# Kernel tuning notes

Measured on AMD Instinct MI355X. Metric: run time of the kernel, lower is better.

The kernel has to match this reference:

```python
import jax, jax.numpy as jnp
import numpy as np

P_THRESHOLD = 0.6
K_CAP = 16


def softmax_m1(x):
    # f(x) = (exp(x)-1) / sum(exp(x)-1), as in the torch module
    fx = jnp.expm1(x)
    return fx / fx.sum(-1, keepdims=True)


def align_chars(start_map, nb_map, max_ch):
    # eval-mode recurrence of NeighborDecoder.align_chars, run for a fixed
    # max_ch steps (no data-dependent early break; char_masks carry the
    # finished state exactly as in torch).
    b = start_map.shape[0]

    def step(carry, i):
        char_map, finished = carry  # [b, N+1], [b] int32
        mask = (finished == 0).astype(char_map.dtype)
        out = (char_map, mask)  # emitted BEFORE the update, matching torch
        finished = finished + (char_map[:, -1] > P_THRESHOLD).astype(jnp.int32)
        kk = jnp.minimum(1 + 2 * i, K_CAP).astype(char_map.dtype)
        cmd = softmax_m1(jax.lax.stop_gradient(char_map) * kk)  # .detach() in torch
        nxt = jnp.einsum('bn,bnm->bm', cmd, nb_map)
        return (nxt, finished), out

    init = (start_map, jnp.zeros(b, jnp.int32))
    _, (maps, masks) = jax.lax.scan(step, init, jnp.arange(max_ch))
    return maps.transpose(1, 0, 2), masks.T  # [b, T, N+1], [b, T]


def setup_inputs() -> dict:
    key = jax.random.key(0)
    ks = jax.random.split(key, 8)
    b, c, h, w = 32, 384, 16, 64
    num_classes = 97
    s = 1.0 / np.sqrt(c)
    return {
        'x': jax.random.normal(ks[0], (b, c, h, w), jnp.float32),
        'eos_emb': (jax.random.normal(ks[1], (c,), jnp.float32) * 0.02),
        'q_w': jax.random.normal(ks[2], (c, c), jnp.float32) * s,
        'q_b': jnp.zeros((c,), jnp.float32),
        'k_w': jax.random.normal(ks[3], (c, c), jnp.float32) * s,
        'k_b': jnp.zeros((c,), jnp.float32),
        'nav_w': jax.random.normal(ks[4], (1, c, c), jnp.float32) * 0.01,
        'nav_b': jnp.zeros((1,), jnp.float32),
        'cls_w': jax.random.normal(ks[5], (num_classes, c), jnp.float32) * s,
        'cls_b': jnp.zeros((num_classes,), jnp.float32),
        'max_char': 48,
    }


def reference(x, eos_emb, q_w, q_b, k_w, k_b, nav_w, nav_b, cls_w, cls_b, max_char):
    b, c, h, w = x.shape
    scale = float(c) ** 0.5
    xt = x.reshape(b, c, h * w).transpose(0, 2, 1)  # [b, N, c]
    g = xt.mean(axis=1)  # [b, c]
    x_ext = jnp.concatenate(
        [xt, jnp.broadcast_to(eos_emb, (b, 1, c))], axis=1)  # [b, N+1, c]

    q_start = g @ q_w.T + q_b                      # [b, c]
    k_feat = x_ext @ k_w.T + k_b                   # [b, N+1, c]
    start_map = jnp.einsum('bnc,bc->bn', k_feat, q_start) / scale
    start_map = jax.nn.softmax(start_map, axis=1)  # [b, N+1]

    q_feat = xt @ q_w.T + q_b                      # [b, N, c]
    # BilinearLayer with out=1: einsum('bim,mn,bjn->bij') + bias
    nb_map = jnp.einsum('bim,mn,bjn->bij', q_feat, nav_w[0], k_feat) + nav_b[0]
    nb_map = jax.nn.softmax(nb_map / scale, axis=2)  # [b, N, N+1]

    last = jnp.zeros((h * w + 1,), x.dtype).at[-1].set(1.0)
    nb_map = jnp.concatenate(
        [nb_map, jnp.broadcast_to(last, (b, 1, h * w + 1))], axis=1)  # [b, N+1, N+1]

    char_maps, char_masks = align_chars(start_map, nb_map, max_char)
    char_feats = jnp.einsum('btn,bnc->btc', char_maps, x_ext)
    char_feats = char_feats * char_masks[..., None]
    logits = char_feats @ cls_w.T + cls_b          # [b, T, num_classes]
    return logits, char_feats, char_maps, char_masks, nb_map
```

## Files before the change

### kernel.cpp

```cpp
#include <hip/hip_runtime.h>
#include <cstdint>
#include <cstddef>

#define BB   32
#define CC   384
#define NN   1024
#define N1   1025
#define TT   48
#define NCLS 97
#define NBL_LD 1088
#define NBTS   1056

static constexpr float INV_SCALE = 1.0f / 19.595917942265423f;

using bf16x8 = __attribute__((ext_vector_type(8))) __bf16;
using f32x4  = __attribute__((ext_vector_type(4))) float;

static constexpr size_t OFF_LOGITS = 0;
static constexpr size_t OFF_CFEAT  = 148992;
static constexpr size_t OFF_CMAPS  = 738816;
static constexpr size_t OFF_CMASK  = 2313216;
static constexpr size_t OFF_NB     = 2314752;

static constexpr size_t OFF_XB     = 0;
static constexpr size_t OFF_WGEM   = 25165824;
static constexpr size_t OFF_BIAS   = 25755648;
static constexpr size_t OFF_G      = 25758720;
static constexpr size_t OFF_QSTART = 25807872;
static constexpr size_t OFF_KEOS   = 25857024;
static constexpr size_t OFF_STATS  = 25858560;
static constexpr size_t OFF_MAPSBF = 26120704;
static constexpr size_t OFF_CMD    = 29266432;
static constexpr size_t OFF_PSUM   = 29536768;
static constexpr size_t OFF_XBT    = 29569536;
static constexpr size_t OFF_NBL    = 29569536;
static constexpr size_t OFF_OUT    = 100942336;
static constexpr size_t OFF_NBT    = 100942336;

__device__ __forceinline__ float bf2f(uint u) {
    union { uint i; float f; } v; v.i = u << 16; return v.f;
}
__device__ __forceinline__ ushort f2bf(float f) {
    union { float f; uint i; } v; v.f = f;
    uint r = v.i + 0x7fffu + ((v.i >> 16) & 1u);
    return (ushort)(r >> 16);
}

__device__ __forceinline__ void gld16(const ushort* g, ushort* l) {
    __builtin_amdgcn_global_load_lds(
        (const __attribute__((address_space(1))) uint*)g,
        (__attribute__((address_space(3))) uint*)l, 16, 0, 0);
}

__global__ __launch_bounds__(256) void k_conv_mean(
    const float* __restrict__ x, ushort* __restrict__ xb, float* __restrict__ g)
{
    int row  = blockIdx.x * 4 + (threadIdx.x >> 6);
    int lane = threadIdx.x & 63;
    const float* src = x + (size_t)row * NN;
    ushort* dst = xb + (size_t)row * NN;
    float s = 0.f;
#pragma unroll
    for (int q = 0; q < 4; q++) {
        float4 v = ((const float4*)src)[q * 64 + lane];
        s += v.x + v.y + v.z + v.w;
        ushort4 p; p.x = f2bf(v.x); p.y = f2bf(v.y); p.z = f2bf(v.z); p.w = f2bf(v.w);
        ((ushort4*)dst)[q * 64 + lane] = p;
    }
#pragma unroll
    for (int o = 32; o; o >>= 1) s += __shfl_down(s, o);
    if (lane == 0) g[row] = s * (1.0f / NN);
}

__global__ __launch_bounds__(256) void k_transpose(
    const ushort* __restrict__ xb, ushort* __restrict__ xbT)
{
    int b = blockIdx.z, c0 = blockIdx.x * 64, n0 = blockIdx.y * 64;
    __shared__ ushort t[64][65];
    int ur = threadIdx.x >> 5, uc = threadIdx.x & 31;
    const ushort* src = xb + ((size_t)b * CC + c0) * NN + n0;
#pragma unroll
    for (int p = 0; p < 8; p++) {
        int c = p * 8 + ur;
        uint v = ((const uint*)(src + (size_t)c * NN))[uc];
        t[c][uc * 2]     = (ushort)(v & 0xffffu);
        t[c][uc * 2 + 1] = (ushort)(v >> 16);
    }
    __syncthreads();
    ushort* dst = xbT + ((size_t)b * N1 + n0) * CC + c0;
#pragma unroll
    for (int p = 0; p < 8; p++) {
        int n = p * 8 + ur;
        uint v = (uint)t[uc * 2][n] | (((uint)t[uc * 2 + 1][n]) << 16);
        ((uint*)(dst + (size_t)n * CC))[uc] = v;
    }
}

__global__ __launch_bounds__(384) void k_setup(
    const float* __restrict__ k_w, const float* __restrict__ k_b,
    const float* __restrict__ nav_w, const float* __restrict__ q_w,
    const float* __restrict__ q_b, const float* __restrict__ eos,
    const float* __restrict__ g,
    ushort* __restrict__ Wgem, float* __restrict__ bias,
    ushort* __restrict__ xbT, float* __restrict__ keos,
    ushort* __restrict__ Out, float* __restrict__ q_start)
{
    int blk = blockIdx.x, c = threadIdx.x;
    if (blk < 384) {
        Wgem[(size_t)blk * CC + c] = f2bf(k_w[(size_t)blk * CC + c]);
        if (c == 0) bias[blk] = k_b[blk];
    } else if (blk < 768) {
        int m = blk - 384;
        float acc = 0.f, accb = 0.f;
        for (int k = 0; k < CC; k++) {
            float nv = nav_w[(size_t)k * CC + m];
            acc  += nv * q_w[(size_t)k * CC + c];
            accb += nv * q_b[k];
        }
        Wgem[(size_t)(CC + m) * CC + c] = f2bf(acc);
        if (c == 0) bias[CC + m] = accb;
    } else if (blk < 800) {
        int b = blk - 768;
        xbT[((size_t)b * N1 + NN) * CC + c] = f2bf(eos[c]);
    } else if (blk == 800) {
        float acc = k_b[c];
        const float* w = k_w + (size_t)c * CC;
        for (int k = 0; k < CC; k++) acc += eos[k] * w[k];
        keos[c] = acc;
        ushort v = f2bf(acc);
        for (int b = 0; b < BB; b++) Out[((size_t)b * N1 + NN) * 768 + c] = v;
    } else {
        int b = blk - 801;
        __shared__ float gs[CC];
        gs[c] = g[(size_t)b * CC + c];
        __syncthreads();
        float acc = q_b[c];
        const float* w = q_w + (size_t)c * CC;
        for (int k = 0; k < CC; k++) acc += gs[k] * w[k];
        q_start[(size_t)b * CC + c] = acc;
    }
}

template<int MODE, int NTN, int PERB>
__global__ __launch_bounds__(256) void k_gemm(
    const ushort* __restrict__ Aall, size_t strideAb, int lda,
    const ushort* __restrict__ Ball, size_t strideBb, int ldb,
    ushort* __restrict__ Cout, size_t strideCb, int ldc,
    const float* __restrict__ bias)
{
    int wid = blockIdx.x;
    int xcd = wid & 7;
    int work = xcd * (PERB * 4) + (wid >> 3);
    int b = work / PERB;
    int r = work - b * PERB;
    int m0 = (r / NTN) * 128, n0 = (r % NTN) * 128;

    const ushort* A  = Aall + (size_t)b * strideAb;
    const ushort* Bp = Ball + (size_t)b * strideBb;
    __shared__ ushort sbuf[16384];
    ushort* As = sbuf;
    ushort* Bs = sbuf + 8192;
    int tid = threadIdx.x, wave = tid >> 6, lane = tid & 63;
    int wm = wave >> 1, wn = wave & 1;
    f32x4 acc[4][4] = {};

    for (int k0 = 0; k0 < CC; k0 += 64) {
#pragma unroll
        for (int q = 0; q < 4; q++) {
            int idx = q * 256 + tid, rr = idx >> 3, sw = idx & 7;
            int src = (sw ^ (rr & 7)) << 3;
            ushort* dA = As + (size_t)(q * 2048 + wave * 512);
            ushort* dB = Bs + (size_t)(q * 2048 + wave * 512);
            gld16(A  + (size_t)(m0 + rr) * lda + k0 + src, dA);
            gld16(Bp + (size_t)(n0 + rr) * ldb + k0 + src, dB);
        }
        __syncthreads();
#pragma unroll
        for (int h = 0; h < 2; h++) {
            bf16x8 af[4], bfr[4];
            int chb = h * 4 + (lane >> 4);
#pragma unroll
            for (int i = 0; i < 4; i++) {
                int row = wm * 64 + i * 16 + (lane & 15);
                af[i]  = *(const bf16x8*)(As + row * 64 + ((chb ^ (row & 7)) << 3));
                int col = wn * 64 + i * 16 + (lane & 15);
                bfr[i] = *(const bf16x8*)(Bs + col * 64 + ((chb ^ (col & 7)) << 3));
            }
#pragma unroll
            for (int i = 0; i < 4; i++)
#pragma unroll
                for (int j = 0; j < 4; j++)
                    acc[i][j] = __builtin_amdgcn_mfma_f32_16x16x32_bf16(af[i], bfr[j], acc[i][j], 0, 0, 0);
        }
        __syncthreads();
    }
#pragma unroll
    for (int i = 0; i < 4; i++) {
        int rl = wm * 64 + i * 16 + ((lane >> 4) << 2);
#pragma unroll
        for (int j = 0; j < 4; j++) {
            int cl = wn * 64 + j * 16 + (lane & 15);
            float bv = (MODE == 0) ? bias[n0 + cl] : 0.f;
#pragma unroll
            for (int rr = 0; rr < 4; rr++) {
                float val = (MODE == 0) ? (acc[i][j][rr] + bv) : (acc[i][j][rr] * INV_SCALE);
                sbuf[(rl + rr) * 128 + cl] = f2bf(val);
            }
        }
    }
    __syncthreads();
    ushort* Cb = Cout + (size_t)b * strideCb;
#pragma unroll
    for (int q = 0; q < 8; q++) {
        int idx = q * 256 + tid, row = idx >> 4, seg = idx & 15;
        *(uint4*)(Cb + (size_t)(m0 + row) * ldc + n0 + seg * 8) =
            *(const uint4*)(sbuf + row * 128 + seg * 8);
    }
}

__global__ __launch_bounds__(1024) void k_start(
    const ushort* __restrict__ Out, const float* __restrict__ q_start,
    float* __restrict__ cmaps)
{
    int b = blockIdx.x, tid = threadIdx.x;
    __shared__ float qs[CC];
    __shared__ float red[16];
    __shared__ float bc;
    if (tid < CC) qs[tid] = q_start[(size_t)b * CC + tid];
    __syncthreads();
    auto dot = [&](int n) {
        const uint4* row = (const uint4*)(Out + ((size_t)b * N1 + n) * 768);
        float acc = 0.f;
        for (int c8 = 0; c8 < CC / 8; c8++) {
            uint4 u = row[c8];
            const ushort* us = (const ushort*)&u;
#pragma unroll
            for (int e = 0; e < 8; e++) acc += bf2f(us[e]) * qs[c8 * 8 + e];
        }
        return acc * INV_SCALE;
    };
    float v0 = dot(tid);
    float v1 = (tid == 0) ? dot(1024) : -1e30f;
    float lm = fmaxf(v0, v1);
#pragma unroll
    for (int o = 32; o; o >>= 1) lm = fmaxf(lm, __shfl_down(lm, o));
    if ((tid & 63) == 0) red[tid >> 6] = lm;
    __syncthreads();
    if (tid == 0) { float m = red[0]; for (int i = 1; i < 16; i++) m = fmaxf(m, red[i]); bc = m; }
    __syncthreads();
    float bmax = bc;
    float e0 = __expf(v0 - bmax);
    float e1 = (tid == 0) ? __expf(v1 - bmax) : 0.f;
    float ls = e0 + e1;
#pragma unroll
    for (int o = 32; o; o >>= 1) ls += __shfl_down(ls, o);
    if ((tid & 63) == 0) red[tid >> 6] = ls;
    __syncthreads();
    if (tid == 0) { float s = 0.f; for (int i = 0; i < 16; i++) s += red[i]; bc = s; }
    __syncthreads();
    float inv = 1.f / bc;
    float* o = cmaps + ((size_t)b * TT) * N1;
    o[tid] = e0 * inv;
    if (tid == 0) o[1024] = e1 * inv;
}

__global__ __launch_bounds__(256) void k_eoscol_nbl(
    const ushort* __restrict__ Out, const float* __restrict__ keos, ushort* __restrict__ nbL)
{
    int gw = blockIdx.x * 4 + (threadIdx.x >> 6);
    int lane = threadIdx.x & 63;
    for (int rr = 0; rr < 4; rr++) {
        int gi = gw * 4 + rr, b = gi >> 10, i = gi & 1023;
        const ushort* row = Out + ((size_t)b * N1 + i) * 768 + 384;
        float acc = 0.f;
        for (int c = lane; c < CC; c += 64) acc += bf2f(row[c]) * keos[c];
#pragma unroll
        for (int o = 32; o; o >>= 1) acc += __shfl_down(acc, o);
        if (lane == 0) nbL[((size_t)b * N1 + i) * NBL_LD + 1024] = f2bf(acc * INV_SCALE);
    }
}

__global__ __launch_bounds__(256) void k_softnb2(
    const ushort* __restrict__ nbL, float* __restrict__ nb, float2* __restrict__ stats)
{
    int bi = blockIdx.x;
    int b = bi >> 10, i = bi & 1023;
    const ushort* row = nbL + ((size_t)b * N1 + i) * NBL_LD;
    int tid = threadIdx.x;
    uint2 u = *(const uint2*)(row + tid * 4);
    float v0 = bf2f(u.x & 0xffffu), v1 = bf2f(u.x >> 16);
    float v2 = bf2f(u.y & 0xffffu), v3 = bf2f(u.y >> 16);
    float vt = (tid == 0) ? bf2f(row[1024]) : -1e30f;
    __shared__ float r1[4]; __shared__ float bc;
    float lm = fmaxf(fmaxf(fmaxf(v0, v1), fmaxf(v2, v3)), vt);
#pragma unroll
    for (int o = 32; o; o >>= 1) lm = fmaxf(lm, __shfl_down(lm, o));
    if ((tid & 63) == 0) r1[tid >> 6] = lm;
    __syncthreads();
    if (tid == 0) bc = fmaxf(fmaxf(r1[0], r1[1]), fmaxf(r1[2], r1[3]));
    __syncthreads();
    float m = bc;
    float e0 = __expf(v0 - m), e1 = __expf(v1 - m), e2 = __expf(v2 - m), e3 = __expf(v3 - m);
    float et = (tid == 0) ? __expf(vt - m) : 0.f;
    float s = e0 + e1 + e2 + e3 + et;
#pragma unroll
    for (int o = 32; o; o >>= 1) s += __shfl_down(s, o);
    if ((tid & 63) == 0) r1[tid >> 6] = s;
    __syncthreads();
    if (tid == 0) bc = r1[0] + r1[1] + r1[2] + r1[3];
    __syncthreads();
    float inv = 1.f / bc;
    float* orow = nb + ((size_t)b * N1 + i) * N1;
    float4 ov = make_float4(e0 * inv, e1 * inv, e2 * inv, e3 * inv);
    *(float4*)(orow + tid * 4) = ov;
    if (tid == 0) { orow[1024] = et * inv; stats[b * 1024 + i] = make_float2(m, inv); }
}

__global__ void k_onehot(float* __restrict__ nb)
{
    int b = blockIdx.x;
    float* row = nb + ((size_t)b * N1 + NN) * N1;
    for (int j = threadIdx.x; j < N1; j += 256)
        row[j] = (j == 1024) ? 1.f : 0.f;
}

__global__ __launch_bounds__(256) void k_transq(
    const ushort* __restrict__ nbL, const float2* __restrict__ stats,
    ushort* __restrict__ nbT)
{
    int b = blockIdx.z, n0 = blockIdx.x * 64, j0 = blockIdx.y * 64;
    __shared__ ushort tile[64][80];
    __shared__ float2 st[64];
    int tid = threadIdx.x;
    if (tid < 64) st[tid] = stats[b * 1024 + n0 + tid];
    __syncthreads();
#pragma unroll
    for (int q = 0; q < 2; q++) {
        int idx = q * 256 + tid, rl = idx >> 3, ch = idx & 7;
        const ushort* src = nbL + ((size_t)b * N1 + n0 + rl) * NBL_LD + j0 + ch * 8;
        uint4 u = *(const uint4*)src;
        float2 s = st[rl];
        const ushort* us = (const ushort*)&u;
#pragma unroll
        for (int k = 0; k < 8; k++)
            tile[ch * 8 + k][rl] = f2bf(__expf(bf2f(us[k]) - s.x) * s.y);
    }
    __syncthreads();
#pragma unroll
    for (int q = 0; q < 2; q++) {
        int idx = q * 256 + tid, jl = idx >> 3, seg = idx & 7;
        int j = j0 + jl;
        if (j <= 1024) {
            uint4 v = *(const uint4*)&tile[jl][seg * 8];
            *(uint4*)(nbT + ((size_t)b * N1 + j) * NBTS + n0 + seg * 8) = v;
        }
    }
}

__global__ __launch_bounds__(256) void k_cmd0(
    const float* __restrict__ cmaps, float* __restrict__ cmd_out, float* __restrict__ ps_out)
{
    int b = blockIdx.x, tid = threadIdx.x;
    __shared__ float red[4];
    const float* m = cmaps + (size_t)b * TT * N1;
    float s = 0.f;
    for (int n = tid; n < N1; n += 256) {
        float c = expm1f(m[n]);
        cmd_out[(size_t)b * 1056 + n] = c;
        s += c;
    }
#pragma unroll
    for (int o = 32; o; o >>= 1) s += __shfl_down(s, o);
    if ((tid & 63) == 0) red[tid >> 6] = s;
    __syncthreads();
    if (tid == 0) ps_out[b * 128] = red[0] + red[1] + red[2] + red[3];
    else if (tid < 128) ps_out[b * 128 + tid] = 0.f;
}

__device__ __forceinline__ float dot16(uint4 r0, uint4 r1,
                                       const float* cA, const float* cB)
{
    const ushort* p0 = (const ushort*)&r0;
    const ushort* p1 = (const ushort*)&r1;
    float acc = 0.f;
#pragma unroll
    for (int e = 0; e < 8; e++) acc += bf2f(p0[e]) * cA[e];
#pragma unroll
    for (int e = 0; e < 8; e++) acc += bf2f(p1[e]) * cB[e];
    return acc;
}

__global__ __launch_bounds__(256) void k_step4(
    float* __restrict__ cmaps, const ushort* __restrict__ nbT,
    const float* __restrict__ cmd_in, float* __restrict__ cmd_out,
    const float* __restrict__ ps_in, float* __restrict__ ps_out, int t)
{
    int b = blockIdx.y, blk = blockIdx.x;
    int tid = threadIdx.x, wave = tid >> 6, lane = tid & 63;
    int j0 = blk * 32 + wave * 8;
    const ushort* base = nbT + (size_t)b * N1 * NBTS;

    uint4 rv[8][2];
#pragma unroll
    for (int r = 0; r < 8; ++r) {
        int j = j0 + r; if (j > 1024) j = 1024;
        const ushort* row = base + (size_t)j * NBTS;
        rv[r][0] = *(const uint4*)(row + lane * 8);
        rv[r][1] = *(const uint4*)(row + 512 + lane * 8);
    }
    const float* ci = cmd_in + (size_t)b * 1056;
    float cA[8], cB[8];
    *(float4*)&cA[0] = *(const float4*)(ci + lane * 8);
    *(float4*)&cA[4] = *(const float4*)(ci + lane * 8 + 4);
    *(float4*)&cB[0] = *(const float4*)(ci + 512 + lane * 8);
    *(float4*)&cB[4] = *(const float4*)(ci + 512 + lane * 8 + 4);
    float ctail = ci[1024];

    __shared__ float sred;
    __shared__ float red[4];
    if (wave == 0) {
        float pv = (lane < 33) ? ps_in[b * 128 + lane] : 0.f;
#pragma unroll
        for (int o = 32; o; o >>= 1) pv += __shfl_down(pv, o);
        if (lane == 0) sred = pv;
    }

    float acc[8];
#pragma unroll
    for (int r = 0; r < 8; ++r) {
        float a = dot16(rv[r][0], rv[r][1], cA, cB);
#pragma unroll
        for (int o = 32; o; o >>= 1) a += __shfl_down(a, o);
        acc[r] = a;
    }
    __syncthreads();
    float inv = 1.f / sred;
    int kkn = 3 + 2 * t; if (kkn > 16) kkn = 16;
    if (lane == 0) {
        float cs = 0.f;
        float* orow = cmaps + ((size_t)b * TT + t + 1) * N1;
        float* co = cmd_out + (size_t)b * 1056;
#pragma unroll
        for (int r = 0; r < 8; ++r) {
            int j = j0 + r;
            if (j <= 1024) {
                float s = acc[r] + ((j == 1024) ? ctail : 0.f);
                float mo = s * inv;
                orow[j] = mo;
                float cn = expm1f((float)kkn * mo);
                co[j] = cn;
                cs += cn;
            }
        }
        red[wave] = cs;
    }
    __syncthreads();
    if (tid == 0)
        ps_out[b * 128 + blk] = red[0] + red[1] + red[2] + red[3];
}

__global__ void k_masks(const float* __restrict__ cmaps, float* __restrict__ cmask)
{
    int b = threadIdx.x;
    if (b < BB) {
        int fin = 0;
        for (int t = 0; t < TT; t++) {
            cmask[b * TT + t] = (fin == 0) ? 1.f : 0.f;
            fin += (cmaps[((size_t)b * TT + t) * N1 + 1024] > 0.6f) ? 1 : 0;
        }
    }
}

__global__ void k_mapsbf(const float* __restrict__ cmaps, ushort* __restrict__ mb)
{
    size_t i = (size_t)blockIdx.x * 256 + threadIdx.x;
    size_t bt = i >> 10; int n = (int)(i & 1023);
    mb[i] = f2bf(cmaps[bt * N1 + n]);
}

__global__ __launch_bounds__(256) void k_cfeat(
    const ushort* __restrict__ mapsbf, const ushort* __restrict__ xb,
    const float* __restrict__ cmaps, const float* __restrict__ eos,
    const float* __restrict__ masks, float* __restrict__ cfeat)
{
    int b = blockIdx.x;
    int wave = threadIdx.x >> 6, lane = threadIdx.x & 63;
    f32x4 acc[3][6] = {};
    const ushort* Ab = mapsbf + (size_t)b * TT * 1024;
    const ushort* Bb = xb + (size_t)b * CC * NN;
    for (int k0 = 0; k0 < NN; k0 += 32) {
        int kk_ = k0 + (lane >> 4) * 8;
        bf16x8 af[3], bfr[6];
#pragma unroll
        for (int i = 0; i < 3; i++)
            af[i] = *(const bf16x8*)(Ab + (size_t)(i * 16 + (lane & 15)) * 1024 + kk_);
#pragma unroll
        for (int j = 0; j < 6; j++)
            bfr[j] = *(const bf16x8*)(Bb + (size_t)(wave * 96 + j * 16 + (lane & 15)) * NN + kk_);
#pragma unroll
        for (int i = 0; i < 3; i++)
#pragma unroll
            for (int j = 0; j < 6; j++)
                acc[i][j] = __builtin_amdgcn_mfma_f32_16x16x32_bf16(af[i], bfr[j], acc[i][j], 0, 0, 0);
    }
#pragma unroll
    for (int i = 0; i < 3; i++) {
        int tbase = i * 16 + ((lane >> 4) << 2);
#pragma unroll
        for (int j = 0; j < 6; j++) {
            int c = wave * 96 + j * 16 + (lane & 15);
            float ev = eos[c];
#pragma unroll
            for (int rr = 0; rr < 4; rr++) {
                int tt = tbase + rr;
                float mlast = cmaps[((size_t)b * TT + tt) * N1 + 1024];
                float val = (acc[i][j][rr] + mlast * ev) * masks[b * TT + tt];
                cfeat[((size_t)b * TT + tt) * CC + c] = val;
            }
        }
    }
}

__global__ __launch_bounds__(128) void k_logits(
    const float* __restrict__ cfeat, const float* __restrict__ cls_w,
    const float* __restrict__ cls_b, float* __restrict__ out)
{
    int bt = blockIdx.x;
    __shared__ float row[CC];
    for (int c = threadIdx.x; c < CC; c += 128) row[c] = cfeat[(size_t)bt * CC + c];
    __syncthreads();
    int j = threadIdx.x;
    if (j < NCLS) {
        float acc = cls_b[j];
        const float* w = cls_w + (size_t)j * CC;
        for (int c = 0; c < CC; c++) acc += row[c] * w[c];
        out[(size_t)bt * NCLS + j] = acc;
    }
}

extern "C" void kernel_launch(void* const* d_in, const int* in_sizes, int n_in,
                              void* d_out, int out_size, void* d_ws, size_t ws_size,
                              hipStream_t stream)
{
    (void)in_sizes; (void)n_in; (void)out_size; (void)ws_size;
    const float* x     = (const float*)d_in[0];
    const float* eos   = (const float*)d_in[1];
    const float* q_w   = (const float*)d_in[2];
    const float* q_b   = (const float*)d_in[3];
    const float* k_w   = (const float*)d_in[4];
    const float* k_b   = (const float*)d_in[5];
    const float* nav_w = (const float*)d_in[6];
    const float* cls_w = (const float*)d_in[8];
    const float* cls_b = (const float*)d_in[9];

    char* ws = (char*)d_ws;
    ushort* xb     = (ushort*)(ws + OFF_XB);
    ushort* Wgem   = (ushort*)(ws + OFF_WGEM);
    float*  bias   = (float*)(ws + OFF_BIAS);
    float*  g      = (float*)(ws + OFF_G);
    float*  qstart = (float*)(ws + OFF_QSTART);
    float*  keos   = (float*)(ws + OFF_KEOS);
    float2* stats  = (float2*)(ws + OFF_STATS);
    ushort* mapsbf = (ushort*)(ws + OFF_MAPSBF);
    float*  cmdbuf = (float*)(ws + OFF_CMD);
    float*  psbuf  = (float*)(ws + OFF_PSUM);
    ushort* xbT    = (ushort*)(ws + OFF_XBT);
    ushort* nbL    = (ushort*)(ws + OFF_NBL);
    ushort* Out    = (ushort*)(ws + OFF_OUT);
    ushort* nbT    = (ushort*)(ws + OFF_NBT);

    float* out     = (float*)d_out;
    float* logits  = out + OFF_LOGITS;
    float* cfeat   = out + OFF_CFEAT;
    float* cmaps   = out + OFF_CMAPS;
    float* cmask   = out + OFF_CMASK;
    float* nb      = out + OFF_NB;

    k_conv_mean<<<3072, 256, 0, stream>>>(x, xb, g);
    k_transpose<<<dim3(6, 16, BB), 256, 0, stream>>>(xb, xbT);
    k_setup<<<833, 384, 0, stream>>>(k_w, k_b, nav_w, q_w, q_b, eos, g,
                                     Wgem, bias, xbT, keos, Out, qstart);

    k_gemm<0, 6, 48><<<1536, 256, 0, stream>>>(
        xbT, (size_t)N1 * CC, CC, Wgem, 0, CC, Out, (size_t)N1 * 768, 768, bias);

    k_start<<<BB, 1024, 0, stream>>>(Out, qstart, cmaps);
    k_cmd0<<<BB, 256, 0, stream>>>(cmaps, cmdbuf, psbuf);
    k_eoscol_nbl<<<2048, 256, 0, stream>>>(Out, keos, nbL);

    k_gemm<1, 8, 64><<<2048, 256, 0, stream>>>(
        Out + 384, (size_t)N1 * 768, 768, Out, (size_t)N1 * 768, 768,
        nbL, (size_t)N1 * NBL_LD, NBL_LD, nullptr);

    k_softnb2<<<BB * NN, 256, 0, stream>>>(nbL, nb, stats);
    k_onehot<<<BB, 256, 0, stream>>>(nb);
    k_transq<<<dim3(16, 17, BB), 256, 0, stream>>>(nbL, stats, nbT);

    for (int t = 0; t < TT - 1; t++)
        k_step4<<<dim3(33, BB), 256, 0, stream>>>(
            cmaps, nbT,
            cmdbuf + (size_t)(t & 1) * 33792, cmdbuf + (size_t)((t + 1) & 1) * 33792,
            psbuf + (size_t)(t & 1) * 4096,  psbuf + (size_t)((t + 1) & 1) * 4096, t);

    k_masks<<<1, 64, 0, stream>>>(cmaps, cmask);
    k_mapsbf<<<6144, 256, 0, stream>>>(cmaps, mapsbf);
    k_cfeat<<<BB, 256, 0, stream>>>(mapsbf, xb, cmaps, eos, cmask, cfeat);
    k_logits<<<BB * TT, 128, 0, stream>>>(cfeat, cls_w, cls_b, logits);
}
```

Baseline: 1.038 ms.

## Replace per-step recurrence launches with persistent kernel using per-batch grid barriers

The 47 per-timestep k_step4 launches are replaced by one persistent kernel, k_rec2, with 256 blocks (8 per batch). Each block keeps its 128 rows of the transposed neighbour map in registers across all steps. Between steps the 8 blocks of a batch synchronise through an atomic counter barrier. Each block recomputes the expm1 weights and their sum from the previous map row held in shared memory, which removes the cmd/partial-sum buffers and the k_cmd0 kernel. This removes launch overhead and the repeated reloading of nbT, but it relies on all 256 blocks being co-resident and adds spin-wait and atomic traffic.

```diff
diff --git a/kernel.cpp b/kernel.cpp
--- a/kernel.cpp
+++ b/kernel.cpp
@@ -30,8 +30,7 @@
 static constexpr size_t OFF_KEOS   = 25857024;
 static constexpr size_t OFF_STATS  = 25858560;
 static constexpr size_t OFF_MAPSBF = 26120704;
-static constexpr size_t OFF_CMD    = 29266432;
-static constexpr size_t OFF_PSUM   = 29536768;
+static constexpr size_t OFF_BAR    = 29266432;
 static constexpr size_t OFF_XBT    = 29569536;
 static constexpr size_t OFF_NBL    = 29569536;
 static constexpr size_t OFF_OUT    = 100942336;
@@ -357,25 +356,7 @@
     }
 }
 
-__global__ __launch_bounds__(256) void k_cmd0(
-    const float* __restrict__ cmaps, float* __restrict__ cmd_out, float* __restrict__ ps_out)
-{
-    int b = blockIdx.x, tid = threadIdx.x;
-    __shared__ float red[4];
-    const float* m = cmaps + (size_t)b * TT * N1;
-    float s = 0.f;
-    for (int n = tid; n < N1; n += 256) {
-        float c = expm1f(m[n]);
-        cmd_out[(size_t)b * 1056 + n] = c;
-        s += c;
-    }
-#pragma unroll
-    for (int o = 32; o; o >>= 1) s += __shfl_down(s, o);
-    if ((tid & 63) == 0) red[tid >> 6] = s;
-    __syncthreads();
-    if (tid == 0) ps_out[b * 128] = red[0] + red[1] + red[2] + red[3];
-    else if (tid < 128) ps_out[b * 128 + tid] = 0.f;
-}
+__global__ void k_barinit(uint* __restrict__ bar) { bar[threadIdx.x] = 0u; }
 
 __device__ __forceinline__ float dot16(uint4 r0, uint4 r1,
                                        const float* cA, const float* cB)
@@ -390,73 +371,95 @@
     return acc;
 }
 
-__global__ __launch_bounds__(256) void k_step4(
-    float* __restrict__ cmaps, const ushort* __restrict__ nbT,
-    const float* __restrict__ cmd_in, float* __restrict__ cmd_out,
-    const float* __restrict__ ps_in, float* __restrict__ ps_out, int t)
-{
-    int b = blockIdx.y, blk = blockIdx.x;
+__global__ __launch_bounds__(512, 2) void k_rec2(
+    float* __restrict__ cmaps, const ushort* __restrict__ nbT, uint* __restrict__ bar)
+{
+    int blk = blockIdx.x;
+    int b = blk >> 3, chunk = blk & 7;
     int tid = threadIdx.x, wave = tid >> 6, lane = tid & 63;
-    int j0 = blk * 32 + wave * 8;
+    int jbase = chunk * 128 + wave * 16;
     const ushort* base = nbT + (size_t)b * N1 * NBTS;
 
-    uint4 rv[8][2];
-#pragma unroll
-    for (int r = 0; r < 8; ++r) {
-        int j = j0 + r; if (j > 1024) j = 1024;
-        const ushort* row = base + (size_t)j * NBTS;
+    uint4 rv[16][2];
+#pragma unroll
+    for (int r = 0; r < 16; ++r) {
+        const ushort* row = base + (size_t)(jbase + r) * NBTS;
         rv[r][0] = *(const uint4*)(row + lane * 8);
         rv[r][1] = *(const uint4*)(row + 512 + lane * 8);
     }
-    const float* ci = cmd_in + (size_t)b * 1056;
-    float cA[8], cB[8];
-    *(float4*)&cA[0] = *(const float4*)(ci + lane * 8);
-    *(float4*)&cA[4] = *(const float4*)(ci + lane * 8 + 4);
-    *(float4*)&cB[0] = *(const float4*)(ci + 512 + lane * 8);
-    *(float4*)&cB[4] = *(const float4*)(ci + 512 + lane * 8 + 4);
-    float ctail = ci[1024];
-
-    __shared__ float sred;
-    __shared__ float red[4];
-    if (wave == 0) {
-        float pv = (lane < 33) ? ps_in[b * 128 + lane] : 0.f;
-#pragma unroll
-        for (int o = 32; o; o >>= 1) pv += __shfl_down(pv, o);
-        if (lane == 0) sred = pv;
-    }
-
-    float acc[8];
-#pragma unroll
-    for (int r = 0; r < 8; ++r) {
-        float a = dot16(rv[r][0], rv[r][1], cA, cB);
-#pragma unroll
-        for (int o = 32; o; o >>= 1) a += __shfl_down(a, o);
-        acc[r] = a;
-    }
-    __syncthreads();
-    float inv = 1.f / sred;
-    int kkn = 3 + 2 * t; if (kkn > 16) kkn = 16;
-    if (lane == 0) {
-        float cs = 0.f;
+    bool hasE = (chunk == 7 && wave == 7);
+    uint4 rvE0 = {}, rvE1 = {};
+    if (hasE) {
+        const ushort* row = base + (size_t)1024 * NBTS;
+        rvE0 = *(const uint4*)(row + lane * 8);
+        rvE1 = *(const uint4*)(row + 512 + lane * 8);
+    }
+
+    __shared__ __align__(16) float cmd[1028];
+    __shared__ float red[8];
+    __shared__ float sinvS;
+
+    for (int t = 0; t < TT - 1; ++t) {
+        const float* mrow = cmaps + ((size_t)b * TT + t) * N1;
+        int kki = 1 + 2 * t; if (kki > 16) kki = 16;
+        float kkf = (float)kki;
+        float m0 = __hip_atomic_load(mrow + tid, __ATOMIC_RELAXED, __HIP_MEMORY_SCOPE_AGENT);
+        float m1 = __hip_atomic_load(mrow + 512 + tid, __ATOMIC_RELAXED, __HIP_MEMORY_SCOPE_AGENT);
+        float c0 = expm1f(kkf * m0), c1 = expm1f(kkf * m1);
+        cmd[tid] = c0; cmd[512 + tid] = c1;
+        float part = c0 + c1;
+        if (tid == 0) {
+            float mt = __hip_atomic_load(mrow + 1024, __ATOMIC_RELAXED, __HIP_MEMORY_SCOPE_AGENT);
+            float ct = expm1f(kkf * mt);
+            cmd[1024] = ct; part += ct;
+        }
+#pragma unroll
+        for (int o = 32; o; o >>= 1) part += __shfl_down(part, o);
+        if (lane == 0) red[wave] = part;
+        __syncthreads();
+        if (tid == 0) {
+            float s = 0.f;
+#pragma unroll
+            for (int w = 0; w < 8; w++) s += red[w];
+            sinvS = 1.f / s;
+        }
+        __syncthreads();
+        float inv = sinvS;
+        float cA[8], cB[8];
+        *(float4*)&cA[0] = *(const float4*)(cmd + lane * 8);
+        *(float4*)&cA[4] = *(const float4*)(cmd + lane * 8 + 4);
+        *(float4*)&cB[0] = *(const float4*)(cmd + 512 + lane * 8);
+        *(float4*)&cB[4] = *(const float4*)(cmd + 512 + lane * 8 + 4);
+        float ctail = cmd[1024];
         float* orow = cmaps + ((size_t)b * TT + t + 1) * N1;
-        float* co = cmd_out + (size_t)b * 1056;
-#pragma unroll
-        for (int r = 0; r < 8; ++r) {
-            int j = j0 + r;
-            if (j <= 1024) {
-                float s = acc[r] + ((j == 1024) ? ctail : 0.f);
-                float mo = s * inv;
-                orow[j] = mo;
-                float cn = expm1f((float)kkn * mo);
-                co[j] = cn;
-                cs += cn;
-            }
-        }
-        red[wave] = cs;
-    }
-    __syncthreads();
-    if (tid == 0)
-        ps_out[b * 128 + blk] = red[0] + red[1] + red[2] + red[3];
+#pragma unroll
+        for (int r = 0; r < 16; ++r) {
+            float a = dot16(rv[r][0], rv[r][1], cA, cB);
+#pragma unroll
+            for (int o = 32; o; o >>= 1) a += __shfl_down(a, o);
+            if (lane == 0)
+                __hip_atomic_store(orow + jbase + r, a * inv,
+                                   __ATOMIC_RELAXED, __HIP_MEMORY_SCOPE_AGENT);
+        }
+        if (hasE) {
+            float a = dot16(rvE0, rvE1, cA, cB);
+#pragma unroll
+            for (int o = 32; o; o >>= 1) a += __shfl_down(a, o);
+            if (lane == 0)
+                __hip_atomic_store(orow + 1024, (a + ctail) * inv,
+                                   __ATOMIC_RELAXED, __HIP_MEMORY_SCOPE_AGENT);
+        }
+        __syncthreads();
+        if (tid == 0) {
+            __builtin_amdgcn_fence(__ATOMIC_RELEASE, "agent");
+            __hip_atomic_fetch_add(&bar[b], 1u, __ATOMIC_RELAXED, __HIP_MEMORY_SCOPE_AGENT);
+            uint want = 8u * (uint)(t + 1);
+            while (__hip_atomic_load(&bar[b], __ATOMIC_RELAXED, __HIP_MEMORY_SCOPE_AGENT) < want)
+                __builtin_amdgcn_s_sleep(2);
+            __builtin_amdgcn_fence(__ATOMIC_ACQUIRE, "agent");
+        }
+        __syncthreads();
+    }
 }
 
 __global__ void k_masks(const float* __restrict__ cmaps, float* __restrict__ cmask)
@@ -562,8 +565,7 @@
     float*  keos   = (float*)(ws + OFF_KEOS);
     float2* stats  = (float2*)(ws + OFF_STATS);
     ushort* mapsbf = (ushort*)(ws + OFF_MAPSBF);
-    float*  cmdbuf = (float*)(ws + OFF_CMD);
-    float*  psbuf  = (float*)(ws + OFF_PSUM);
+    uint*   bar    = (uint*)(ws + OFF_BAR);
     ushort* xbT    = (ushort*)(ws + OFF_XBT);
     ushort* nbL    = (ushort*)(ws + OFF_NBL);
     ushort* Out    = (ushort*)(ws + OFF_OUT);
@@ -580,12 +582,12 @@
     k_transpose<<<dim3(6, 16, BB), 256, 0, stream>>>(xb, xbT);
     k_setup<<<833, 384, 0, stream>>>(k_w, k_b, nav_w, q_w, q_b, eos, g,
                                      Wgem, bias, xbT, keos, Out, qstart);
+    k_barinit<<<1, 32, 0, stream>>>(bar);
 
     k_gemm<0, 6, 48><<<1536, 256, 0, stream>>>(
         xbT, (size_t)N1 * CC, CC, Wgem, 0, CC, Out, (size_t)N1 * 768, 768, bias);
 
     k_start<<<BB, 1024, 0, stream>>>(Out, qstart, cmaps);
-    k_cmd0<<<BB, 256, 0, stream>>>(cmaps, cmdbuf, psbuf);
     k_eoscol_nbl<<<2048, 256, 0, stream>>>(Out, keos, nbL);
 
     k_gemm<1, 8, 64><<<2048, 256, 0, stream>>>(
@@ -596,11 +598,7 @@
     k_onehot<<<BB, 256, 0, stream>>>(nb);
     k_transq<<<dim3(16, 17, BB), 256, 0, stream>>>(nbL, stats, nbT);
 
-    for (int t = 0; t < TT - 1; t++)
-        k_step4<<<dim3(33, BB), 256, 0, stream>>>(
-            cmaps, nbT,
-            cmdbuf + (size_t)(t & 1) * 33792, cmdbuf + (size_t)((t + 1) & 1) * 33792,
-            psbuf + (size_t)(t & 1) * 4096,  psbuf + (size_t)((t + 1) & 1) * 4096, t);
+    k_rec2<<<256, 512, 0, stream>>>(cmaps, nbT, bar);
 
     k_masks<<<1, 64, 0, stream>>>(cmaps, cmask);
     k_mapsbf<<<6144, 256, 0, stream>>>(cmaps, mapsbf);
```

New measurement: 1.306 ms. 1.26x slower.

## Quantize transposed neighbor map to int8 with per-row scales for recurrence steps

Applied to the files above, without the earlier changes.

Adds a one-time kernel that converts the bf16 transposed neighbor matrix to uint8 with a per-row max-based scale. The 47 recurrence step kernels then read half as many bytes per step, applying the scale after the dot product. Each block now covers 64 rows instead of 32, so the partial-sum reduction handles 17 entries. This trades a small extra quantization pass and reduced numerical precision (about 1/254 of the row max) for lower memory traffic in the bandwidth-bound loop.

```diff
diff --git a/kernel.cpp b/kernel.cpp
--- a/kernel.cpp
+++ b/kernel.cpp
@@ -10,6 +10,7 @@
 #define NCLS 97
 #define NBL_LD 1088
 #define NBTS   1056
+#define NBQS   1056
 
 static constexpr float INV_SCALE = 1.0f / 19.595917942265423f;
 
@@ -34,6 +35,8 @@
 static constexpr size_t OFF_PSUM   = 29536768;
 static constexpr size_t OFF_XBT    = 29569536;
 static constexpr size_t OFF_NBL    = 29569536;
+static constexpr size_t OFF_NBQ    = 29569536;
+static constexpr size_t OFF_SCL    = 64206336;
 static constexpr size_t OFF_OUT    = 100942336;
 static constexpr size_t OFF_NBT    = 100942336;
 
@@ -357,6 +360,45 @@
     }
 }
 
+__global__ __launch_bounds__(256) void k_quant(
+    const ushort* __restrict__ nbT, unsigned char* __restrict__ nbQ,
+    float* __restrict__ scl)
+{
+    int b = blockIdx.y;
+    int j = blockIdx.x * 4 + (threadIdx.x >> 6);
+    int lane = threadIdx.x & 63;
+    if (j > 1024) return;
+    const ushort* row = nbT + ((size_t)b * N1 + j) * NBTS;
+    uint4 v0 = *(const uint4*)(row + lane * 16);
+    uint4 v1 = *(const uint4*)(row + lane * 16 + 8);
+    const ushort* u0 = (const ushort*)&v0;
+    const ushort* u1 = (const ushort*)&v1;
+    float p[16];
+#pragma unroll
+    for (int e = 0; e < 8; ++e) { p[e] = bf2f(u0[e]); p[8 + e] = bf2f(u1[e]); }
+    float m = 0.f;
+#pragma unroll
+    for (int e = 0; e < 16; ++e) m = fmaxf(m, p[e]);
+#pragma unroll
+    for (int o = 32; o; o >>= 1) m = fmaxf(m, __shfl_xor(m, o));
+    m = fmaxf(m, 1e-20f);
+    float rcp = 127.f / m;
+    uint w[4];
+#pragma unroll
+    for (int q = 0; q < 4; ++q) {
+        uint r = 0;
+#pragma unroll
+        for (int k = 0; k < 4; ++k) {
+            uint qv = (uint)(p[q * 4 + k] * rcp + 0.5f);
+            r |= qv << (8 * k);
+        }
+        w[q] = r;
+    }
+    *(uint4*)(nbQ + ((size_t)b * N1 + j) * NBQS + lane * 16) =
+        make_uint4(w[0], w[1], w[2], w[3]);
+    if (lane == 0) scl[(size_t)b * 1056 + j] = m * (1.f / 127.f);
+}
+
 __global__ __launch_bounds__(256) void k_cmd0(
     const float* __restrict__ cmaps, float* __restrict__ cmd_out, float* __restrict__ ps_out)
 {
@@ -377,58 +419,52 @@
     else if (tid < 128) ps_out[b * 128 + tid] = 0.f;
 }
 
-__device__ __forceinline__ float dot16(uint4 r0, uint4 r1,
-                                       const float* cA, const float* cB)
-{
-    const ushort* p0 = (const ushort*)&r0;
-    const ushort* p1 = (const ushort*)&r1;
-    float acc = 0.f;
-#pragma unroll
-    for (int e = 0; e < 8; e++) acc += bf2f(p0[e]) * cA[e];
-#pragma unroll
-    for (int e = 0; e < 8; e++) acc += bf2f(p1[e]) * cB[e];
-    return acc;
-}
-
-__global__ __launch_bounds__(256) void k_step4(
-    float* __restrict__ cmaps, const ushort* __restrict__ nbT,
+__global__ __launch_bounds__(256) void k_step5(
+    float* __restrict__ cmaps, const unsigned char* __restrict__ nbQ,
+    const float* __restrict__ scl,
     const float* __restrict__ cmd_in, float* __restrict__ cmd_out,
     const float* __restrict__ ps_in, float* __restrict__ ps_out, int t)
 {
     int b = blockIdx.y, blk = blockIdx.x;
     int tid = threadIdx.x, wave = tid >> 6, lane = tid & 63;
-    int j0 = blk * 32 + wave * 8;
-    const ushort* base = nbT + (size_t)b * N1 * NBTS;
-
-    uint4 rv[8][2];
-#pragma unroll
-    for (int r = 0; r < 8; ++r) {
+    int j0 = blk * 64 + wave * 16;
+    const unsigned char* base = nbQ + (size_t)b * N1 * NBQS;
+
+    uint4 rv[16];
+#pragma unroll
+    for (int r = 0; r < 16; ++r) {
         int j = j0 + r; if (j > 1024) j = 1024;
-        const ushort* row = base + (size_t)j * NBTS;
-        rv[r][0] = *(const uint4*)(row + lane * 8);
-        rv[r][1] = *(const uint4*)(row + 512 + lane * 8);
+        rv[r] = *(const uint4*)(base + (size_t)j * NBQS + lane * 16);
     }
     const float* ci = cmd_in + (size_t)b * 1056;
-    float cA[8], cB[8];
-    *(float4*)&cA[0] = *(const float4*)(ci + lane * 8);
-    *(float4*)&cA[4] = *(const float4*)(ci + lane * 8 + 4);
-    *(float4*)&cB[0] = *(const float4*)(ci + 512 + lane * 8);
-    *(float4*)&cB[4] = *(const float4*)(ci + 512 + lane * 8 + 4);
+    float cC[16];
+#pragma unroll
+    for (int q = 0; q < 4; ++q)
+        *(float4*)&cC[q * 4] = *(const float4*)(ci + lane * 16 + q * 4);
     float ctail = ci[1024];
 
     __shared__ float sred;
     __shared__ float red[4];
     if (wave == 0) {
-        float pv = (lane < 33) ? ps_in[b * 128 + lane] : 0.f;
-#pragma unroll
-        for (int o = 32; o; o >>= 1) pv += __shfl_down(pv, o);
+        float pv = (lane < 17) ? ps_in[b * 128 + lane] : 0.f;
+#pragma unroll
+        for (int o = 16; o; o >>= 1) pv += __shfl_down(pv, o);
         if (lane == 0) sred = pv;
     }
 
-    float acc[8];
-#pragma unroll
-    for (int r = 0; r < 8; ++r) {
-        float a = dot16(rv[r][0], rv[r][1], cA, cB);
+    float acc[16];
+#pragma unroll
+    for (int r = 0; r < 16; ++r) {
+        float a = 0.f;
+        const uint* w = (const uint*)&rv[r];
+#pragma unroll
+        for (int q = 0; q < 4; ++q) {
+            uint v = w[q];
+            a += (float)(v & 255u)         * cC[q * 4 + 0];
+            a += (float)((v >> 8) & 255u)  * cC[q * 4 + 1];
+            a += (float)((v >> 16) & 255u) * cC[q * 4 + 2];
+            a += (float)(v >> 24)          * cC[q * 4 + 3];
+        }
 #pragma unroll
         for (int o = 32; o; o >>= 1) a += __shfl_down(a, o);
         acc[r] = a;
@@ -440,11 +476,12 @@
         float cs = 0.f;
         float* orow = cmaps + ((size_t)b * TT + t + 1) * N1;
         float* co = cmd_out + (size_t)b * 1056;
-#pragma unroll
-        for (int r = 0; r < 8; ++r) {
+        const float* sc = scl + (size_t)b * 1056;
+#pragma unroll
+        for (int r = 0; r < 16; ++r) {
             int j = j0 + r;
             if (j <= 1024) {
-                float s = acc[r] + ((j == 1024) ? ctail : 0.f);
+                float s = acc[r] * sc[j] + ((j == 1024) ? ctail : 0.f);
                 float mo = s * inv;
                 orow[j] = mo;
                 float cn = expm1f((float)kkn * mo);
@@ -566,6 +603,8 @@
     float*  psbuf  = (float*)(ws + OFF_PSUM);
     ushort* xbT    = (ushort*)(ws + OFF_XBT);
     ushort* nbL    = (ushort*)(ws + OFF_NBL);
+    unsigned char* nbQ = (unsigned char*)(ws + OFF_NBQ);
+    float*  scl    = (float*)(ws + OFF_SCL);
     ushort* Out    = (ushort*)(ws + OFF_OUT);
     ushort* nbT    = (ushort*)(ws + OFF_NBT);
 
@@ -595,10 +634,11 @@
     k_softnb2<<<BB * NN, 256, 0, stream>>>(nbL, nb, stats);
     k_onehot<<<BB, 256, 0, stream>>>(nb);
     k_transq<<<dim3(16, 17, BB), 256, 0, stream>>>(nbL, stats, nbT);
+    k_quant<<<dim3(257, BB), 256, 0, stream>>>(nbT, nbQ, scl);
 
     for (int t = 0; t < TT - 1; t++)
-        k_step4<<<dim3(33, BB), 256, 0, stream>>>(
-            cmaps, nbT,
+        k_step5<<<dim3(17, BB), 256, 0, stream>>>(
+            cmaps, nbQ, scl,
             cmdbuf + (size_t)(t & 1) * 33792, cmdbuf + (size_t)((t + 1) & 1) * 33792,
             psbuf + (size_t)(t & 1) * 4096,  psbuf + (size_t)((t + 1) & 1) * 4096, t);
 
```

Measured after the change: 1.004 ms. -3.3%, faster.
